# Kernel tuning notes

Hardware: AMD Instinct MI355X
Metric: run time of the kernel (lower is better)

Reference implementation:

```python
import jax, jax.numpy as jnp
import numpy as np

D_MODEL = 1024
NUM_HEADS = 16
D_K = D_MODEL // NUM_HEADS
B, S = 2, 2048


def setup_inputs() -> dict:
    key = jax.random.key(0)
    ks = jax.random.split(key, 9)
    scale = 1.0 / np.sqrt(D_MODEL)
    return {
        "hidden_states": jax.random.normal(ks[0], (B, S, D_MODEL), dtype=jnp.float32),
        "attention_mask": jnp.ones((B, S, S), dtype=jnp.int32),
        "Wq": jax.random.normal(ks[1], (D_MODEL, D_MODEL), dtype=jnp.float32) * scale,
        "bq": jnp.zeros((D_MODEL,), dtype=jnp.float32),
        "Wk": jax.random.normal(ks[2], (D_MODEL, D_MODEL), dtype=jnp.float32) * scale,
        "bk": jnp.zeros((D_MODEL,), dtype=jnp.float32),
        "Wv": jax.random.normal(ks[3], (D_MODEL, D_MODEL), dtype=jnp.float32) * scale,
        "bv": jnp.zeros((D_MODEL,), dtype=jnp.float32),
        "Wo": jax.random.normal(ks[4], (D_MODEL, D_MODEL), dtype=jnp.float32) * scale,
        "bo": jnp.zeros((D_MODEL,), dtype=jnp.float32),
    }


def reference(hidden_states, attention_mask, Wq, bq, Wk, bk, Wv, bv, Wo, bo):
    b, s, _ = hidden_states.shape
    # torch Linear: y = x @ W.T + b
    def proj(W, bias):
        y = jnp.einsum('bsd,ed->bse', hidden_states, W) + bias
        return y.reshape(b, s, NUM_HEADS, D_K).transpose(0, 2, 1, 3)  # [B,H,S,dk]
    q = proj(Wq, bq)
    k = proj(Wk, bk)
    v = proj(Wv, bv)
    scores = jnp.einsum('bnqd,bnkd->bnqk', q, k) / np.sqrt(D_K)
    mask = attention_mask[:, None, :, :]  # [B,1,S,S]
    scores = jnp.where(mask == 0, jnp.float32(-1e9), scores)
    attn = jax.nn.softmax(scores, axis=-1)  # dropout = identity (eval)
    ctx = jnp.einsum('bnqk,bnkd->bnqd', attn, v)
    ctx = ctx.transpose(0, 2, 1, 3).reshape(b, s, D_MODEL)
    return jnp.einsum('bsd,ed->bse', ctx, Wo) + bo
```

## Files before the change

kernel.cpp:

```cpp
#include <hip/hip_runtime.h>

typedef short short8 __attribute__((ext_vector_type(8)));
typedef float floatx4 __attribute__((ext_vector_type(4)));
typedef float floatx16 __attribute__((ext_vector_type(16)));
typedef unsigned short ushort4v __attribute__((ext_vector_type(4)));

#define DEV static __device__ __forceinline__

DEV unsigned short f2bf(float f) {
  unsigned int u = __builtin_bit_cast(unsigned int, f);
  u += 0x7fffu + ((u >> 16) & 1u);
  return (unsigned short)(u >> 16);
}

DEV unsigned int cvtpk(float a, float b) {
  unsigned int r;
  asm("v_cvt_pk_bf16_f32 %0, %1, %2" : "=v"(r) : "v"(a), "v"(b));
  return r;
}

DEV void gload16(const unsigned short* g, unsigned short* l) {
  __builtin_amdgcn_global_load_lds((__attribute__((address_space(1))) void*)g,
                                   (__attribute__((address_space(3))) void*)l,
                                   16, 0, 0);
}

__global__ void convert_kernel(const float* __restrict__ hs, const float* __restrict__ Wq,
                               const float* __restrict__ Wk, const float* __restrict__ Wv,
                               const float* __restrict__ Wo,
                               unsigned short* __restrict__ xbf, unsigned short* __restrict__ wqkv,
                               unsigned short* __restrict__ wobf,
                               const int* __restrict__ mask, unsigned long long* __restrict__ bits) {
  if (blockIdx.x >= 8192) {
    int w = (blockIdx.x - 8192) * 256 + threadIdx.x;
    const int4* p = (const int4*)(mask + (size_t)w * 64);
    unsigned long long r = 0ull;
#pragma unroll
    for (int j = 0; j < 16; ++j) {
      int4 m = p[j];
      r |= (unsigned long long)(m.x != 0) << (j * 4 + 0);
      r |= (unsigned long long)(m.y != 0) << (j * 4 + 1);
      r |= (unsigned long long)(m.z != 0) << (j * 4 + 2);
      r |= (unsigned long long)(m.w != 0) << (j * 4 + 3);
    }
    bits[w] = r;
    return;
  }
  size_t i4 = ((size_t)blockIdx.x * 256 + threadIdx.x) * 4;
  const float* src;
  unsigned short* dst;
  if (i4 < 4194304) {
    src = hs + i4; dst = xbf + i4;
  } else if (i4 < 7340032) {
    size_t o = i4 - 4194304;
    size_t lo = o & 1048575;
    src = (o < 1048576) ? (Wq + lo) : ((o < 2097152) ? (Wk + lo) : (Wv + lo));
    dst = wqkv + o;
  } else {
    size_t o = i4 - 7340032;
    src = Wo + o; dst = wobf + o;
  }
  float4 v = *(const float4*)src;
  ushort4v u;
  u.x = f2bf(v.x); u.y = f2bf(v.y); u.z = f2bf(v.z); u.w = f2bf(v.w);
  *(ushort4v*)dst = u;
}

__global__ void __launch_bounds__(256, 2) qkv_gemm(
    const unsigned short* __restrict__ X, const unsigned short* __restrict__ W,
    const float* __restrict__ bq, const float* __restrict__ bk, const float* __restrict__ bv,
    unsigned short* __restrict__ Qb, unsigned short* __restrict__ Kb,
    unsigned short* __restrict__ Vt) {
  __shared__ __align__(16) unsigned short As[128 * 32];
  __shared__ __align__(16) unsigned short Bs[128 * 32];
  const int tid = threadIdx.x;
  const int lane = tid & 63, wv = tid >> 6;
  const int wm = wv >> 1, wn = wv & 1;
  const int quad = lane >> 4, l15 = lane & 15;
  const int mb = blockIdx.y, nb = blockIdx.x;
  const bool sw = (nb < 16);

  const unsigned short* ga = X + (size_t)(mb * 128 + (tid >> 2)) * 1024 + (tid & 3) * 8;
  const unsigned short* gb = W + (size_t)(nb * 128 + (tid >> 2)) * 1024 + (tid & 3) * 8;
  unsigned short* la1 = As + tid * 8;
  unsigned short* la2 = As + 2048 + tid * 8;
  unsigned short* lb1 = Bs + tid * 8;
  unsigned short* lb2 = Bs + 2048 + tid * 8;

  const int wx = sw ? wn : wm;
  const int ww = sw ? wm : wn;

  floatx4 acc[4][4] = {};
  for (int kt = 0; kt < 32; ++kt) {
    const int k0 = kt * 32;
    gload16(ga + k0, la1);
    gload16(ga + k0 + 65536, la2);
    gload16(gb + k0, lb1);
    gload16(gb + k0 + 65536, lb2);
    __syncthreads();
    short8 xa[4], wb[4];
#pragma unroll
    for (int i = 0; i < 4; ++i) {
      xa[i] = *(const short8*)&As[(wx * 64 + i * 16 + l15) * 32 + quad * 8];
      wb[i] = *(const short8*)&Bs[(ww * 64 + i * 16 + l15) * 32 + quad * 8];
    }
    if (sw) {
#pragma unroll
      for (int mt = 0; mt < 4; ++mt)
#pragma unroll
        for (int nt = 0; nt < 4; ++nt)
          acc[mt][nt] = __builtin_amdgcn_mfma_f32_16x16x32_bf16(wb[mt], xa[nt], acc[mt][nt], 0, 0, 0);
    } else {
#pragma unroll
      for (int mt = 0; mt < 4; ++mt)
#pragma unroll
        for (int nt = 0; nt < 4; ++nt)
          acc[mt][nt] = __builtin_amdgcn_mfma_f32_16x16x32_bf16(xa[mt], wb[nt], acc[mt][nt], 0, 0, 0);
    }
    __syncthreads();
  }

  if (sw) {
#pragma unroll
    for (int mt = 0; mt < 4; ++mt) {
      const int wc0 = nb * 128 + wm * 64 + mt * 16 + quad * 4;
      const int mat = wc0 >> 10;
      const int nl0 = wc0 & 1023;
      const int hh = nl0 >> 6, d0 = nl0 & 63;
      const float4 b4 = *(const float4*)((mat ? bk : bq) + nl0);
      const float fac = mat ? 1.0f : 0.18033688011112042f;
#pragma unroll
      for (int nt = 0; nt < 4; ++nt) {
        const int colx = mb * 128 + wn * 64 + nt * 16 + l15;
        const int bb = colx >> 11, s = colx & 2047;
        ushort4v pv;
        pv[0] = f2bf((acc[mt][nt][0] + b4.x) * fac);
        pv[1] = f2bf((acc[mt][nt][1] + b4.y) * fac);
        pv[2] = f2bf((acc[mt][nt][2] + b4.z) * fac);
        pv[3] = f2bf((acc[mt][nt][3] + b4.w) * fac);
        if (mat == 0) {
          *(ushort4v*)&Qb[((size_t)(bb * 16 + hh) * 2048 + s) * 64 + d0] = pv;
        } else {
          const size_t idx = (size_t)(bb * 16 + hh) * 131072 + (s >> 5) * 2048 +
                             (d0 >> 4) * 512 + (((d0 >> 3) & 1) * 32 + (s & 31)) * 8 + (d0 & 7);
          *(ushort4v*)&Kb[idx] = pv;
        }
      }
    }
  } else {
#pragma unroll
    for (int nt = 0; nt < 4; ++nt) {
      const int col = nb * 128 + wn * 64 + nt * 16 + l15;
      const int nl = col & 1023;
      const float bias = bv[nl];
      const int hh = nl >> 6, d = nl & 63;
#pragma unroll
      for (int mt = 0; mt < 4; ++mt) {
        const int row0 = mb * 128 + wm * 64 + mt * 16 + quad * 4;
        const int bb = row0 >> 11, s0 = row0 & 2047;
        ushort4v pv;
#pragma unroll
        for (int r = 0; r < 4; ++r) pv[r] = f2bf(acc[mt][nt][r] + bias);
        const size_t idx = (size_t)(bb * 16 + hh) * 131072 + (s0 >> 5) * 2048 +
                           ((s0 >> 4) & 1) * 1024 + (d >> 5) * 512 +
                           (((s0 >> 3) & 1) * 32 + (d & 31)) * 8 + (s0 & 7);
        *(ushort4v*)&Vt[idx] = pv;
      }
    }
  }
}

__global__ void __launch_bounds__(256, 2) attn_kernel(
    const unsigned short* __restrict__ Qb, const unsigned short* __restrict__ Kb,
    const unsigned short* __restrict__ Vt, const unsigned long long* __restrict__ mbits,
    unsigned short* __restrict__ ctx) {
  __shared__ float red[2 * 64 * 33];
  const int tid = threadIdx.x;
  const int lane = tid & 63, wv = tid >> 6;
  const int l31 = lane & 31, h = lane >> 5;
  const int qg = wv & 1, h2 = wv >> 1;
  const int bid = (blockIdx.x & 7) * 128 + (blockIdx.x >> 3);
  const int pair = bid >> 5, qt = bid & 31;
  const int b_ = pair >> 4, hd = pair & 15;
  const int qrow = qt * 64 + qg * 32 + l31;

  short8 qf[4];
#pragma unroll
  for (int ks = 0; ks < 4; ++ks)
    qf[ks] = *(const short8*)(Qb + (size_t)pair * 131072 + (size_t)qrow * 64 + ks * 16 + h * 8);

  const unsigned short* kp = Kb + (size_t)pair * 131072 + h2 * 65536 + lane * 8;
  const unsigned short* vp = Vt + (size_t)pair * 131072 + h2 * 65536 + lane * 8;

  const unsigned long long* mrow = mbits + ((size_t)b_ * 2048 + qrow) * 32 + h2 * 16;

  short8 kf[4], vf[4];
#pragma unroll
  for (int i = 0; i < 4; ++i) kf[i] = *(const short8*)(kp + i * 512);
#pragma unroll
  for (int i = 0; i < 4; ++i) vf[i] = *(const short8*)(vp + i * 512);

  floatx16 acc_o[2] = {};
  const floatx16 Zv = {};
  float lsum = 0.f;

#pragma unroll 2
  for (int it = 0; it < 32; ++it) {
    const unsigned long long w = mrow[it >> 1];
    const int bitbase = (it & 1) * 32;

    __builtin_amdgcn_s_setprio(1);
    floatx16 accs = __builtin_amdgcn_mfma_f32_32x32x16_bf16(kf[0], qf[0], Zv, 0, 0, 0);
#pragma unroll
    for (int ks = 1; ks < 4; ++ks)
      accs = __builtin_amdgcn_mfma_f32_32x32x16_bf16(kf[ks], qf[ks], accs, 0, 0, 0);
    __builtin_amdgcn_s_setprio(0);

    kp += 2048;
#pragma unroll
    for (int i = 0; i < 4; ++i) kf[i] = *(const short8*)(kp + i * 512);

    if (__any(w != ~0ull)) {
#pragma unroll
      for (int reg = 0; reg < 16; ++reg) {
        const int kl = (reg & 3) + 8 * (reg >> 2) + 4 * h;
        if (!((w >> (bitbase + kl)) & 1ull)) accs[reg] = -6e9f;
      }
    }

    unsigned int pk[8];
    float ls0 = 0.f, ls1 = 0.f;
#pragma unroll
    for (int i = 0; i < 8; ++i) {
      const float a = exp2f(accs[2 * i]);
      const float b = exp2f(accs[2 * i + 1]);
      ls0 += a;
      ls1 += b;
      pk[i] = cvtpk(a, b);
    }
    lsum += ls0 + ls1;
#pragma unroll
    for (int u = 0; u < 2; ++u) {
      auto r02 = __builtin_amdgcn_permlane32_swap(pk[4 * u + 0], pk[4 * u + 2], false, false);
      auto r13 = __builtin_amdgcn_permlane32_swap(pk[4 * u + 1], pk[4 * u + 3], false, false);
      union { unsigned int wd[4]; short8 s8; } af;
      af.wd[0] = r02[0];
      af.wd[1] = r13[0];
      af.wd[2] = r02[1];
      af.wd[3] = r13[1];
      __builtin_amdgcn_s_setprio(1);
#pragma unroll
      for (int nt = 0; nt < 2; ++nt)
        acc_o[nt] = __builtin_amdgcn_mfma_f32_32x32x16_bf16(af.s8, vf[u * 2 + nt], acc_o[nt], 0, 0, 0);
      __builtin_amdgcn_s_setprio(0);
    }

    vp += 2048;
#pragma unroll
    for (int i = 0; i < 4; ++i) vf[i] = *(const short8*)(vp + i * 512);
  }

  lsum += __shfl_xor(lsum, 32);

  if (h2 == 1) {
    float* p = red + (qg * 64 + lane) * 33;
#pragma unroll
    for (int reg = 0; reg < 16; ++reg) {
      p[reg] = acc_o[0][reg];
      p[16 + reg] = acc_o[1][reg];
    }
    p[32] = lsum;
  }
  __syncthreads();
  if (h2 == 0) {
    const float* p = red + (qg * 64 + lane) * 33;
#pragma unroll
    for (int reg = 0; reg < 16; ++reg) {
      acc_o[0][reg] += p[reg];
      acc_o[1][reg] += p[16 + reg];
    }
    lsum += p[32];
    const float rinv = 1.f / ((lsum > 0.f) ? lsum : 1.f);
#pragma unroll
    for (int reg = 0; reg < 16; ++reg) {
      const int ql = (reg & 3) + 8 * (reg >> 2) + 4 * h;
      const float rl = __shfl(rinv, ql);
      const size_t base = ((size_t)b_ * 2048 + qt * 64 + qg * 32 + ql) * 1024 + hd * 64;
      ctx[base + l31]      = f2bf(acc_o[0][reg] * rl);
      ctx[base + 32 + l31] = f2bf(acc_o[1][reg] * rl);
    }
  }
}

__global__ void __launch_bounds__(256, 2) out_gemm(
    const unsigned short* __restrict__ C, const unsigned short* __restrict__ W,
    const float* __restrict__ bo, float* __restrict__ out) {
  __shared__ __align__(16) unsigned short As[128 * 32];
  __shared__ __align__(16) unsigned short Bs[64 * 32];
  const int tid = threadIdx.x;
  const int lane = tid & 63, wv = tid >> 6;
  const int wm = wv >> 1, wn = wv & 1;
  const int quad = lane >> 4, l15 = lane & 15;
  const int mb = blockIdx.y, nb = blockIdx.x;

  const unsigned short* ga = C + (size_t)(mb * 128 + (tid >> 2)) * 1024 + (tid & 3) * 8;
  const unsigned short* gb = W + (size_t)(nb * 64 + (tid >> 2)) * 1024 + (tid & 3) * 8;
  unsigned short* la1 = As + tid * 8;
  unsigned short* la2 = As + 2048 + tid * 8;
  unsigned short* lb1 = Bs + tid * 8;

  floatx4 acc[4][2] = {};
  for (int kt = 0; kt < 32; ++kt) {
    const int k0 = kt * 32;
    gload16(ga + k0, la1);
    gload16(ga + k0 + 65536, la2);
    gload16(gb + k0, lb1);
    __syncthreads();
    short8 af[4], bfr[2];
#pragma unroll
    for (int i = 0; i < 4; ++i)
      af[i] = *(const short8*)&As[(wm * 64 + i * 16 + l15) * 32 + quad * 8];
#pragma unroll
    for (int i = 0; i < 2; ++i)
      bfr[i] = *(const short8*)&Bs[(wn * 32 + i * 16 + l15) * 32 + quad * 8];
#pragma unroll
    for (int mt = 0; mt < 4; ++mt)
#pragma unroll
      for (int nt = 0; nt < 2; ++nt)
        acc[mt][nt] = __builtin_amdgcn_mfma_f32_16x16x32_bf16(af[mt], bfr[nt], acc[mt][nt], 0, 0, 0);
    __syncthreads();
  }
#pragma unroll
  for (int nt = 0; nt < 2; ++nt) {
    const int col = nb * 64 + wn * 32 + nt * 16 + l15;
    const float bias = bo[col];
#pragma unroll
    for (int mt = 0; mt < 4; ++mt)
#pragma unroll
      for (int r = 0; r < 4; ++r) {
        const int row = mb * 128 + wm * 64 + mt * 16 + quad * 4 + r;
        out[(size_t)row * 1024 + col] = acc[mt][nt][r] + bias;
      }
  }
}

extern "C" void kernel_launch(void* const* d_in, const int* in_sizes, int n_in,
                              void* d_out, int out_size, void* d_ws, size_t ws_size,
                              hipStream_t stream) {
  const float* hs = (const float*)d_in[0];
  const int* mask = (const int*)d_in[1];
  const float* Wq = (const float*)d_in[2];
  const float* bq = (const float*)d_in[3];
  const float* Wk = (const float*)d_in[4];
  const float* bk = (const float*)d_in[5];
  const float* Wv = (const float*)d_in[6];
  const float* bv = (const float*)d_in[7];
  const float* Wo = (const float*)d_in[8];
  const float* bo = (const float*)d_in[9];
  float* out = (float*)d_out;

  char* ws = (char*)d_ws;
  unsigned short* xbf  = (unsigned short*)(ws + 0);
  unsigned short* wqkv = (unsigned short*)(ws + 8388608);
  unsigned short* wobf = (unsigned short*)(ws + 14680064);
  unsigned short* Qb   = (unsigned short*)(ws + 16777216);
  unsigned short* Kb   = (unsigned short*)(ws + 25165824);
  unsigned short* Vt   = (unsigned short*)(ws + 33554432);
  unsigned short* ctx  = (unsigned short*)(ws + 41943040);
  unsigned long long* mbits = (unsigned long long*)(ws + 50331648);

  convert_kernel<<<8704, 256, 0, stream>>>(hs, Wq, Wk, Wv, Wo, xbf, wqkv, wobf, mask, mbits);
  qkv_gemm<<<dim3(24, 32), 256, 0, stream>>>(xbf, wqkv, bq, bk, bv, Qb, Kb, Vt);
  attn_kernel<<<1024, 256, 0, stream>>>(Qb, Kb, Vt, mbits, ctx);
  out_gemm<<<dim3(16, 32), 256, 0, stream>>>(ctx, wobf, bo, out);
}
```

Baseline: 252.3 us.

## Pre-swizzle X and QKV weights into MFMA fragment order; load fragments directly from global

The fp32-to-bf16 conversion kernel now writes hidden states and the QKV weights in a tiled layout that matches the MFMA operand fragment order. The QKV GEMM drops its LDS staging and barriers, with each wave reading its fragments straight from global memory using coalesced 16-byte loads. The next k-step's loads are issued after the current MFMAs as simple register prefetching. This removes LDS traffic and syncs, but operands shared across waves are now fetched separately by each wave through cache, and there is only one stage of prefetch to hide global latency.

Result: faster. 246.8 us (-2.2%).

```diff
diff --git a/kernel.cpp b/kernel.cpp
--- a/kernel.cpp
+++ b/kernel.cpp
@@ -50,12 +50,19 @@
   const float* src;
   unsigned short* dst;
   if (i4 < 4194304) {
-    src = hs + i4; dst = xbf + i4;
+    const int r = (int)(i4 >> 10), c = (int)(i4 & 1023);
+    src = hs + i4;
+    const int p = r >> 6, fi = (r & 63) >> 4, l15f = r & 15;
+    const int ktc = c >> 5, qdc = (c >> 3) & 3, e = c & 7;
+    dst = xbf + ((size_t)(p * 128 + ktc * 4 + fi) * 512 + (qdc * 16 + l15f) * 8 + e);
   } else if (i4 < 7340032) {
     size_t o = i4 - 4194304;
     size_t lo = o & 1048575;
     src = (o < 1048576) ? (Wq + lo) : ((o < 2097152) ? (Wk + lo) : (Wv + lo));
-    dst = wqkv + o;
+    const int r = (int)(o >> 10), c = (int)(o & 1023);
+    const int p = r >> 6, fi = (r & 63) >> 4, l15f = r & 15;
+    const int ktc = c >> 5, qdc = (c >> 3) & 3, e = c & 7;
+    dst = wqkv + ((size_t)(p * 128 + ktc * 4 + fi) * 512 + (qdc * 16 + l15f) * 8 + e);
   } else {
     size_t o = i4 - 7340032;
     src = Wo + o; dst = wobf + o;
@@ -67,12 +74,10 @@
 }
 
 __global__ void __launch_bounds__(256, 2) qkv_gemm(
-    const unsigned short* __restrict__ X, const unsigned short* __restrict__ W,
+    const unsigned short* __restrict__ Xf, const unsigned short* __restrict__ Wf,
     const float* __restrict__ bq, const float* __restrict__ bk, const float* __restrict__ bv,
     unsigned short* __restrict__ Qb, unsigned short* __restrict__ Kb,
     unsigned short* __restrict__ Vt) {
-  __shared__ __align__(16) unsigned short As[128 * 32];
-  __shared__ __align__(16) unsigned short Bs[128 * 32];
   const int tid = threadIdx.x;
   const int lane = tid & 63, wv = tid >> 6;
   const int wm = wv >> 1, wn = wv & 1;
@@ -80,30 +85,20 @@
   const int mb = blockIdx.y, nb = blockIdx.x;
   const bool sw = (nb < 16);
 
-  const unsigned short* ga = X + (size_t)(mb * 128 + (tid >> 2)) * 1024 + (tid & 3) * 8;
-  const unsigned short* gb = W + (size_t)(nb * 128 + (tid >> 2)) * 1024 + (tid & 3) * 8;
-  unsigned short* la1 = As + tid * 8;
-  unsigned short* la2 = As + 2048 + tid * 8;
-  unsigned short* lb1 = Bs + tid * 8;
-  unsigned short* lb2 = Bs + 2048 + tid * 8;
-
   const int wx = sw ? wn : wm;
   const int ww = sw ? wm : wn;
 
+  const unsigned short* xp = Xf + (size_t)(mb * 2 + wx) * 65536 + lane * 8;
+  const unsigned short* wp = Wf + (size_t)(nb * 2 + ww) * 65536 + lane * 8;
+
+  short8 xa[4], wb[4];
+#pragma unroll
+  for (int i = 0; i < 4; ++i) xa[i] = *(const short8*)(xp + i * 512);
+#pragma unroll
+  for (int i = 0; i < 4; ++i) wb[i] = *(const short8*)(wp + i * 512);
+
   floatx4 acc[4][4] = {};
   for (int kt = 0; kt < 32; ++kt) {
-    const int k0 = kt * 32;
-    gload16(ga + k0, la1);
-    gload16(ga + k0 + 65536, la2);
-    gload16(gb + k0, lb1);
-    gload16(gb + k0 + 65536, lb2);
-    __syncthreads();
-    short8 xa[4], wb[4];
-#pragma unroll
-    for (int i = 0; i < 4; ++i) {
-      xa[i] = *(const short8*)&As[(wx * 64 + i * 16 + l15) * 32 + quad * 8];
-      wb[i] = *(const short8*)&Bs[(ww * 64 + i * 16 + l15) * 32 + quad * 8];
-    }
     if (sw) {
 #pragma unroll
       for (int mt = 0; mt < 4; ++mt)
@@ -117,7 +112,13 @@
         for (int nt = 0; nt < 4; ++nt)
           acc[mt][nt] = __builtin_amdgcn_mfma_f32_16x16x32_bf16(xa[mt], wb[nt], acc[mt][nt], 0, 0, 0);
     }
-    __syncthreads();
+    xp += 2048; wp += 2048;
+    if (kt < 31) {
+#pragma unroll
+      for (int i = 0; i < 4; ++i) xa[i] = *(const short8*)(xp + i * 512);
+#pragma unroll
+      for (int i = 0; i < 4; ++i) wb[i] = *(const short8*)(wp + i * 512);
+    }
   }
 
   if (sw) {
```
